# Performance work log

Hardware: AMD Instinct MI355X
Metric: run time of the kernel (lower is better)

Reference implementation:

```python
import jax, jax.numpy as jnp
import numpy as np

NUM_HEADS = 16
CLAMP = 1e4


def setup_inputs() -> dict:
    key = jax.random.key(0)
    ks = jax.random.split(key, 8)
    B, Nq, Nkv, Cq, Ckv = 4, 2048, 2048, 1024, 768
    s_q = 1.0 / np.sqrt(Cq)
    s_kv = 1.0 / np.sqrt(Ckv)
    return {
        "query": jax.random.normal(ks[0], (B, Nq, Cq), jnp.float32),
        "key_value": jax.random.normal(ks[1], (B, Nkv, Ckv), jnp.float32),
        "Wq": jax.random.normal(ks[2], (Cq, Cq), jnp.float32) * s_q,
        "bq": jnp.zeros((Cq,), jnp.float32),
        "Wk": jax.random.normal(ks[3], (Ckv, Cq), jnp.float32) * s_kv,
        "bk": jnp.zeros((Cq,), jnp.float32),
        "Wv": jax.random.normal(ks[4], (Ckv, Cq), jnp.float32) * s_kv,
        "bv": jnp.zeros((Cq,), jnp.float32),
        "Wo": jax.random.normal(ks[5], (Cq, Cq), jnp.float32) * s_q,
        "bo": jnp.zeros((Cq,), jnp.float32),
    }


def reference(query, key_value, Wq, bq, Wk, bk, Wv, bv, Wo, bo):
    B, Nq, Cq = query.shape
    Nkv = key_value.shape[1]
    H = NUM_HEADS
    D = Cq // H
    scale = D ** (-0.5)

    # projections -> [B, H, N, D]
    q = (query @ Wq + bq).reshape(B, Nq, H, D).transpose(0, 2, 1, 3)
    k = (key_value @ Wk + bk).reshape(B, Nkv, H, D).transpose(0, 2, 1, 3)
    v = (key_value @ Wv + bv).reshape(B, Nkv, H, D).transpose(0, 2, 1, 3)

    # scores [B, H, Nq, Nkv] with clamp (mask=None path)
    attn = jnp.einsum("bhqd,bhkd->bhqk", q, k) * scale
    attn = jnp.clip(attn, -CLAMP, CLAMP)
    attn = jax.nn.softmax(attn, axis=-1)
    # NaN fallback: replace with uniform attention if any NaN present
    attn = jnp.where(jnp.any(jnp.isnan(attn)),
                     jnp.asarray(1.0 / Nkv, attn.dtype), attn)

    # weighted sum -> [B, Nq, Cq]
    x = jnp.einsum("bhqk,bhkd->bqhd", attn, v).reshape(B, Nq, Cq)
    return x @ Wo + bo
```

## Files before the change

### kernel.cpp

```cpp
#include <hip/hip_runtime.h>
#include <hip/hip_bf16.h>
#include <stdint.h>


typedef unsigned short u16;
typedef __attribute__((ext_vector_type(2))) float f32x2;
typedef __attribute__((ext_vector_type(4))) short bf16x4;
typedef __attribute__((ext_vector_type(8))) short bf16x8;
typedef __attribute__((ext_vector_type(4))) float f32x4;
typedef __attribute__((ext_vector_type(16))) float f32x16;

__device__ __forceinline__ u16 f2bf(float x) {
  union { float f; uint32_t u; } c; c.f = x;
  uint32_t r = c.u + 0x7fffu + ((c.u >> 16) & 1u);
  return (u16)(r >> 16);
}

__device__ __forceinline__ uint32_t pkbf(float a, float b) {
#if __has_builtin(__builtin_amdgcn_cvt_pk_bf16_f32)
  typedef __attribute__((ext_vector_type(2))) __bf16 bf2;
  bf2 r = __builtin_amdgcn_cvt_pk_bf16_f32(a, b);
  return __builtin_bit_cast(uint32_t, r);
#else
  return (uint32_t)f2bf(a) | ((uint32_t)f2bf(b) << 16);
#endif
}

__device__ __forceinline__ void gld16(const void* g, void* l) {
  __builtin_amdgcn_global_load_lds(
      (const __attribute__((address_space(1))) void*)g,
      (__attribute__((address_space(3))) void*)l, 16, 0, 0);
}

__device__ __forceinline__ void cvt_body(const float* __restrict__ in,
                                         u16* __restrict__ out, int blk) {
  int i = (blk * 256 + threadIdx.x) * 8;
  float4 a = *(const float4*)(in + i);
  float4 b = *(const float4*)(in + i + 4);
  union { u16 u[8]; uint4 v; } o;
  o.u[0] = f2bf(a.x); o.u[1] = f2bf(a.y); o.u[2] = f2bf(a.z); o.u[3] = f2bf(a.w);
  o.u[4] = f2bf(b.x); o.u[5] = f2bf(b.y); o.u[6] = f2bf(b.z); o.u[7] = f2bf(b.w);
  *(uint4*)(out + i) = o.v;
}

__device__ __forceinline__ void transpose_body(const float* __restrict__ in,
                                               u16* __restrict__ out,
                                               int R, int C, int bx, int by) {
  __shared__ float tile[64][65];
  int c0 = bx * 64, r0 = by * 64;
  #pragma unroll
  for (int it = 0; it < 16; it++) {
    int idx = threadIdx.x + it * 256;
    int lr = idx >> 6, lc = idx & 63;
    tile[lr][lc] = in[(size_t)(r0 + lr) * C + c0 + lc];
  }
  __syncthreads();
  #pragma unroll
  for (int it = 0; it < 16; it++) {
    int idx = threadIdx.x + it * 256;
    int lc = idx >> 6, lr = idx & 63;
    out[(size_t)(c0 + lc) * R + r0 + lr] = f2bf(tile[lr][lc]);
  }
}

__global__ void prep_kernel(const float* __restrict__ query,
                            const float* __restrict__ key_value,
                            const float* __restrict__ Wq, const float* __restrict__ Wk,
                            const float* __restrict__ Wv, const float* __restrict__ Wo,
                            u16* qb, u16* kvb, u16* WqT, u16* WkT, u16* WvT, u16* WoT) {
  int blk = blockIdx.x;
  if (blk < 4096) { cvt_body(query, qb, blk); return; }
  if (blk < 7168) { cvt_body(key_value, kvb, blk - 4096); return; }
  if (blk < 7424) { int lo = blk - 7168; transpose_body(Wq, WqT, 1024, 1024, lo & 15, lo >> 4); return; }
  if (blk < 7616) { int lo = blk - 7424; transpose_body(Wk, WkT, 768, 1024, lo & 15, lo >> 4); return; }
  if (blk < 7808) { int lo = blk - 7616; transpose_body(Wv, WvT, 768, 1024, lo & 15, lo >> 4); return; }
  { int lo = blk - 7808; transpose_body(Wo, WoT, 1024, 1024, lo & 15, lo >> 4); return; }
}

template<bool SWAP>
__device__ __forceinline__ void gemm_kloop(const u16* __restrict__ A,
                                           const u16* __restrict__ BT,
                                           int K, char* smem, f32x4 (&acc)[4][4],
                                           int m0, int n0, int tid) {
  const u16* ap[4]; const u16* bp[4]; int ldA[4], ldB[4];
  #pragma unroll
  for (int it2 = 0; it2 < 4; it2++) {
    int s = it2 * 256 + tid;
    int row = s >> 3, cl = (s & 7) ^ (row & 7);
    ap[it2] = A + (size_t)(m0 + row) * K + cl * 8;
    bp[it2] = BT + (size_t)(n0 + row) * K + cl * 8;
    ldA[it2] = s * 16;
    ldB[it2] = 16384 + s * 16;
  }
  const int w = tid >> 6, l = tid & 63;
  const int lm = l & 15, lq = l >> 4;
  const int wr = w >> 1, wc = w & 1;
  int abase[4], bbase[4];
  #pragma unroll
  for (int i = 0; i < 4; i++) {
    int m = wr * 64 + i * 16 + lm;
    abase[i] = m * 128 + ((lq ^ (m & 7)) << 4);
    int n = wc * 64 + i * 16 + lm;
    bbase[i] = 16384 + n * 128 + ((lq ^ (n & 7)) << 4);
  }
  for (int k0 = 0; k0 < K; k0 += 64) {
    #pragma unroll
    for (int it2 = 0; it2 < 4; it2++) {
      gld16(ap[it2], smem + ldA[it2]);
      gld16(bp[it2], smem + ldB[it2]);
      ap[it2] += 64; bp[it2] += 64;
    }
    __syncthreads();
    #pragma unroll
    for (int kk = 0; kk < 2; kk++) {
      bf16x8 af[4], bf[4];
      #pragma unroll
      for (int i = 0; i < 4; i++)
        af[i] = *(const bf16x8*)(smem + (abase[i] ^ (kk << 6)));
      #pragma unroll
      for (int j = 0; j < 4; j++)
        bf[j] = *(const bf16x8*)(smem + (bbase[j] ^ (kk << 6)));
      #pragma unroll
      for (int i = 0; i < 4; i++)
        #pragma unroll
        for (int j = 0; j < 4; j++) {
          if (SWAP)
            acc[i][j] = __builtin_amdgcn_mfma_f32_16x16x32_bf16(bf[j], af[i], acc[i][j], 0, 0, 0);
          else
            acc[i][j] = __builtin_amdgcn_mfma_f32_16x16x32_bf16(af[i], bf[j], acc[i][j], 0, 0, 0);
        }
    }
    __syncthreads();
  }
}

__global__ __launch_bounds__(256, 3)
void gemm_qkv(const u16* __restrict__ qb, const u16* __restrict__ kvb,
              const u16* __restrict__ WqT, const u16* __restrict__ WkT,
              const u16* __restrict__ WvT,
              const float* __restrict__ bq, const float* __restrict__ bk,
              const float* __restrict__ bv,
              u16* __restrict__ Qb, u16* __restrict__ Kbf, u16* __restrict__ Vt,
              float qscale) {
  extern __shared__ __align__(16) char smem[];
  const int tid = threadIdx.x;
  const int w = tid >> 6, l = tid & 63;
  const int lm = l & 15, lq = l >> 4;
  const int m0 = blockIdx.y * 128, n0 = blockIdx.x * 128;
  const int wr = w >> 1, wc = w & 1;
  const int z = blockIdx.z;
  f32x4 acc[4][4] = {};

  u16* etile = (u16*)(smem + w * 9216);
  const int xr = l >> 3, cc = (l & 7) ^ xr;

  if (z < 2) {
    const u16* A = (z == 0) ? qb : kvb;
    const u16* BT = (z == 0) ? WqT : WkT;
    const float* bias = (z == 0) ? bq : bk;
    u16* out = (z == 0) ? Qb : Kbf;
    const float scale = (z == 0) ? qscale : 1.0f;
    const int K = (z == 0) ? 1024 : 768;
    gemm_kloop<true>(A, BT, K, smem, acc, m0, n0, tid);
    #pragma unroll
    for (int j = 0; j < 4; j++) {
      float4 b4 = *(const float4*)&bias[n0 + wc * 64 + j * 16 + lq * 4];
      #pragma unroll
      for (int i = 0; i < 4; i++) {
        uint2 pkd;
        pkd.x = pkbf((acc[i][j][0] + b4.x) * scale, (acc[i][j][1] + b4.y) * scale);
        pkd.y = pkbf((acc[i][j][2] + b4.z) * scale, (acc[i][j][3] + b4.w) * scale);
        *(uint2*)&etile[(i * 16 + lm) * 72 + j * 16 + lq * 4] = pkd;
      }
    }
    u16* gbase = out + (size_t)(m0 + wr * 64) * 1024 + n0 + wc * 64;
    #pragma unroll
    for (int co = 0; co < 8; co++) {
      int ml = co * 8 + xr;
      uint4 d = *(const uint4*)&etile[ml * 72 + cc * 8];
      *(uint4*)&gbase[(size_t)ml * 1024 + cc * 8] = d;
    }
  } else {
    gemm_kloop<false>(kvb, WvT, 768, smem, acc, m0, n0, tid);
    #pragma unroll
    for (int j = 0; j < 4; j++) {
      float bi = bv[n0 + wc * 64 + j * 16 + lm];
      #pragma unroll
      for (int i = 0; i < 4; i++) {
        uint2 pkd;
        pkd.x = pkbf(acc[i][j][0] + bi, acc[i][j][1] + bi);
        pkd.y = pkbf(acc[i][j][2] + bi, acc[i][j][3] + bi);
        *(uint2*)&etile[(j * 16 + lm) * 72 + i * 16 + lq * 4] = pkd;
      }
    }
    const int bb = m0 >> 11, mloc = (m0 & 2047) + wr * 64;
    u16* gbase = Vt + ((size_t)bb * 1024 + n0 + wc * 64) * 2048 + mloc;
    const int kvA = (cc >> 1) * 16 + (cc & 1) * 4;
    #pragma unroll
    for (int co = 0; co < 8; co++) {
      int dl = co * 8 + xr;
      uint2 dA = *(const uint2*)&etile[dl * 72 + kvA];
      uint2 dB = *(const uint2*)&etile[dl * 72 + kvA + 8];
      uint4 d = {dA.x, dA.y, dB.x, dB.y};
      *(uint4*)&gbase[(size_t)dl * 2048 + cc * 8] = d;
    }
  }
}

__global__ __launch_bounds__(256, 3)
void gemm_o(const u16* __restrict__ A, const u16* __restrict__ BT,
            const float* __restrict__ bias, float* __restrict__ Cout) {
  __shared__ __align__(16) char smem[32768];
  const int tid = threadIdx.x;
  const int w = tid >> 6, l = tid & 63;
  const int lm = l & 15, lq = l >> 4;
  const int m0 = blockIdx.y * 128, n0 = blockIdx.x * 128;
  const int wr = w >> 1, wc = w & 1;
  f32x4 acc[4][4] = {};
  gemm_kloop<false>(A, BT, 1024, smem, acc, m0, n0, tid);
  #pragma unroll
  for (int j = 0; j < 4; j++) {
    int gn = n0 + wc * 64 + j * 16 + lm;
    float bi = bias[gn];
    #pragma unroll
    for (int i = 0; i < 4; i++) {
      int gm = m0 + wr * 64 + i * 16 + lq * 4;
      #pragma unroll
      for (int r = 0; r < 4; r++)
        Cout[(size_t)(gm + r) * 1024 + gn] = acc[i][j][r] + bi;
    }
  }
}

__global__ __launch_bounds__(256, 2)
void attn_kernel(const u16* __restrict__ Q, const u16* __restrict__ Kb,
                 const u16* __restrict__ Vt, u16* __restrict__ X) {
  __shared__ __align__(16) char smem[32768];
  const int tid = threadIdx.x, w = tid >> 6, l = tid & 63;
  const int l31 = l & 31, h5 = l >> 5;
  const int bh = blockIdx.x, b = bh >> 4, h = bh & 15;
  const int q0 = blockIdx.y * 256 + w * 64;
  const int rx = l31 & 7;

  const u16* Kg = Kb + (size_t)b * 2048 * 1024 + h * 64;
  const u16* Vg = Vt + (size_t)bh * 64 * 2048;

  const u16 *kp0, *kp1, *vp0, *vp1;
  {
    int s = tid, r = s >> 3, c = (s & 7) ^ (r & 7);
    kp0 = Kg + (size_t)r * 1024 + c * 8;
    vp0 = Vg + (size_t)r * 2048 + c * 8;
    s = 256 + tid; r = s >> 3; c = (s & 7) ^ (r & 7);
    kp1 = Kg + (size_t)r * 1024 + c * 8;
    vp1 = Vg + (size_t)r * 2048 + c * 8;
  }
  const int kd0 = tid * 16, kd1 = (256 + tid) * 16;

  bf16x8 qfA[4], qfB[4];
  {
    const u16* qp = Q + ((size_t)(b * 2048 + q0 + l31)) * 1024 + h * 64 + h5 * 8;
    #pragma unroll
    for (int t = 0; t < 4; t++) qfA[t] = *(const bf16x8*)(qp + t * 16);
    qp += (size_t)32 * 1024;
    #pragma unroll
    for (int t = 0; t < 4; t++) qfB[t] = *(const bf16x8*)(qp + t * 16);
  }

  const int kvb2 = (l31 << 7) | ((rx ^ h5) << 4);
  const int vb2 = 16384 | (l31 << 7) | ((rx ^ h5) << 4);

  f32x16 xaccA[2] = {}, xaccB[2] = {};
  f32x2 lsA = {0.f, 0.f}, lsB = {0.f, 0.f};
  const f32x16 KZ = {};

  gld16(kp0, smem + kd0); gld16(kp1, smem + kd1);
  gld16(vp0, smem + 16384 + kd0); gld16(vp1, smem + 16384 + kd1);
  kp0 += 65536; kp1 += 65536; vp0 += 64; vp1 += 64;
  __syncthreads();

#define ATTN_STEP(CUR, DOPREF)                                                  \
  {                                                                             \
    if (DOPREF) {                                                               \
      const int nb = ((CUR) ^ 1) << 13;                                         \
      gld16(kp0, smem + nb + kd0); gld16(kp1, smem + nb + kd1);                 \
      gld16(vp0, smem + 16384 + nb + kd0); gld16(vp1, smem + 16384 + nb + kd1); \
      kp0 += 65536; kp1 += 65536; vp0 += 64; vp1 += 64;                         \
    }                                                                           \
    _Pragma("unroll")                                                           \
    for (int sub = 0; sub < 2; sub++) {                                         \
      const int km = ((CUR) << 13) | (sub << 12);                               \
      bf16x8 kf[4];                                                             \
      _Pragma("unroll")                                                         \
      for (int t = 0; t < 4; t++)                                               \
        kf[t] = *(const bf16x8*)(smem + (kvb2 ^ (km | (t << 5))));              \
      f32x16 st = __builtin_amdgcn_mfma_f32_32x32x16_bf16(kf[0], qfA[0], KZ, 0, 0, 0); \
      _Pragma("unroll")                                                         \
      for (int t = 1; t < 4; t++)                                               \
        st = __builtin_amdgcn_mfma_f32_32x32x16_bf16(kf[t], qfA[t], st, 0, 0, 0); \
      uint32_t pkA[8], pkB[8];                                                  \
      _Pragma("unroll")                                                         \
      for (int u = 0; u < 4; u++) {                                             \
        float p0 = __builtin_amdgcn_exp2f(st[4 * u + 0]);                       \
        float p1 = __builtin_amdgcn_exp2f(st[4 * u + 1]);                       \
        float p2 = __builtin_amdgcn_exp2f(st[4 * u + 2]);                       \
        float p3 = __builtin_amdgcn_exp2f(st[4 * u + 3]);                       \
        lsA += (f32x2){p0 + p2, p1 + p3};                                       \
        pkA[2 * u] = pkbf(p0, p1); pkA[2 * u + 1] = pkbf(p2, p3);               \
      }                                                                         \
      st = __builtin_amdgcn_mfma_f32_32x32x16_bf16(kf[0], qfB[0], KZ, 0, 0, 0); \
      _Pragma("unroll")                                                         \
      for (int t = 1; t < 4; t++)                                               \
        st = __builtin_amdgcn_mfma_f32_32x32x16_bf16(kf[t], qfB[t], st, 0, 0, 0); \
      _Pragma("unroll")                                                         \
      for (int u = 0; u < 4; u++) {                                             \
        float p0 = __builtin_amdgcn_exp2f(st[4 * u + 0]);                       \
        float p1 = __builtin_amdgcn_exp2f(st[4 * u + 1]);                       \
        float p2 = __builtin_amdgcn_exp2f(st[4 * u + 2]);                       \
        float p3 = __builtin_amdgcn_exp2f(st[4 * u + 3]);                       \
        lsB += (f32x2){p0 + p2, p1 + p3};                                       \
        pkB[2 * u] = pkbf(p0, p1); pkB[2 * u + 1] = pkbf(p2, p3);               \
      }                                                                         \
      _Pragma("unroll")                                                         \
      for (int c2 = 0; c2 < 2; c2++) {                                          \
        union { uint32_t d[4]; bf16x8 v; } pfA, pfB;                            \
        _Pragma("unroll")                                                       \
        for (int dd = 0; dd < 4; dd++) {                                        \
          pfA.d[dd] = pkA[4 * c2 + dd]; pfB.d[dd] = pkB[4 * c2 + dd];           \
        }                                                                       \
        const int vx = ((sub << 2) | (c2 << 1)) << 4;                           \
        _Pragma("unroll")                                                       \
        for (int dt = 0; dt < 2; dt++) {                                        \
          bf16x8 vf = *(const bf16x8*)(smem +                                   \
              (vb2 ^ (((CUR) << 13) | (dt << 12) | vx)));                       \
          xaccA[dt] = __builtin_amdgcn_mfma_f32_32x32x16_bf16(vf, pfA.v, xaccA[dt], 0, 0, 0); \
          xaccB[dt] = __builtin_amdgcn_mfma_f32_32x32x16_bf16(vf, pfB.v, xaccB[dt], 0, 0, 0); \
        }                                                                       \
      }                                                                         \
    }                                                                           \
    __syncthreads();                                                            \
  }

  for (int itp = 0; itp < 15; itp++) {
    ATTN_STEP(0, true)
    ATTN_STEP(1, true)
  }
  ATTN_STEP(0, true)
  ATTN_STEP(1, false)
#undef ATTN_STEP

  {
    float lsum = lsA[0] + lsA[1];
    const float inv = 1.0f / (lsum + __shfl_xor(lsum, 32));
    u16* xp = X + ((size_t)(b * 2048 + q0 + l31)) * 1024 + h * 64;
    #pragma unroll
    for (int dt = 0; dt < 2; dt++)
      #pragma unroll
      for (int g = 0; g < 4; g++) {
        const int d0 = dt * 32 + g * 8 + h5 * 4;
        uint2 o;
        o.x = pkbf(xaccA[dt][4 * g + 0] * inv, xaccA[dt][4 * g + 1] * inv);
        o.y = pkbf(xaccA[dt][4 * g + 2] * inv, xaccA[dt][4 * g + 3] * inv);
        *(uint2*)(xp + d0) = o;
      }
  }
  {
    float lsum = lsB[0] + lsB[1];
    const float inv = 1.0f / (lsum + __shfl_xor(lsum, 32));
    u16* xp = X + ((size_t)(b * 2048 + q0 + 32 + l31)) * 1024 + h * 64;
    #pragma unroll
    for (int dt = 0; dt < 2; dt++)
      #pragma unroll
      for (int g = 0; g < 4; g++) {
        const int d0 = dt * 32 + g * 8 + h5 * 4;
        uint2 o;
        o.x = pkbf(xaccB[dt][4 * g + 0] * inv, xaccB[dt][4 * g + 1] * inv);
        o.y = pkbf(xaccB[dt][4 * g + 2] * inv, xaccB[dt][4 * g + 3] * inv);
        *(uint2*)(xp + d0) = o;
      }
  }
}

extern "C" void kernel_launch(void* const* d_in, const int* in_sizes, int n_in,
                              void* d_out, int out_size, void* d_ws, size_t ws_size,
                              hipStream_t stream) {
  const float* query     = (const float*)d_in[0];
  const float* key_value = (const float*)d_in[1];
  const float* Wq = (const float*)d_in[2];
  const float* bq = (const float*)d_in[3];
  const float* Wk = (const float*)d_in[4];
  const float* bk = (const float*)d_in[5];
  const float* Wv = (const float*)d_in[6];
  const float* bv = (const float*)d_in[7];
  const float* Wo = (const float*)d_in[8];
  const float* bo = (const float*)d_in[9];
  float* out = (float*)d_out;

  char* ws = (char*)d_ws;
  size_t off = 0;
  auto alloc = [&](size_t bytes) -> void* {
    void* p = ws + off; off += (bytes + 255) & ~(size_t)255; return p;
  };
  u16* qb  = (u16*)alloc((size_t)8192 * 1024 * 2);
  u16* kvb = (u16*)alloc((size_t)8192 * 768 * 2);
  u16* WqT = (u16*)alloc((size_t)1024 * 1024 * 2);
  u16* WkT = (u16*)alloc((size_t)1024 * 768 * 2);
  u16* WvT = (u16*)alloc((size_t)1024 * 768 * 2);
  u16* WoT = (u16*)alloc((size_t)1024 * 1024 * 2);
  u16* Qb  = (u16*)alloc((size_t)8192 * 1024 * 2);
  u16* Kbf = (u16*)alloc((size_t)8192 * 1024 * 2);
  u16* Vt  = (u16*)alloc((size_t)8192 * 1024 * 2);
  u16* Xb  = (u16*)alloc((size_t)8192 * 1024 * 2);

  prep_kernel<<<8064, 256, 0, stream>>>(query, key_value, Wq, Wk, Wv, Wo,
                                        qb, kvb, WqT, WkT, WvT, WoT);

  const float qscale = 0.125f * 1.4426950408889634f;
  gemm_qkv<<<dim3(8, 64, 3), 256, 36864, stream>>>(qb, kvb, WqT, WkT, WvT,
                                                   bq, bk, bv, Qb, Kbf, Vt, qscale);

  attn_kernel<<<dim3(64, 8), 256, 0, stream>>>(Qb, Kbf, Vt, Xb);

  gemm_o<<<dim3(8, 64), 256, 0, stream>>>(Xb, WoT, bo, out);
}
```

Before: 291.0 us.

## Store K/V in MFMA fragment layout and load attention operands directly to registers

The QKV GEMM epilogue now writes K and V in a per-head, fragment-ordered layout so each lane can read its MFMA operand with contiguous 16-byte global loads. The attention kernel drops its shared-memory staging, LDS swizzle and per-step barriers, and instead double-buffers K/V fragments in registers with a software-prefetched global load of the next tile. Each wave now fetches K/V independently from global or L2, where before they were shared through LDS. Register pressure also rises.

```diff
diff --git a/kernel.cpp b/kernel.cpp
--- a/kernel.cpp
+++ b/kernel.cpp
@@ -140,7 +140,7 @@
               const u16* __restrict__ WvT,
               const float* __restrict__ bq, const float* __restrict__ bk,
               const float* __restrict__ bv,
-              u16* __restrict__ Qb, u16* __restrict__ Kbf, u16* __restrict__ Vt,
+              u16* __restrict__ Qb, u16* __restrict__ Kf, u16* __restrict__ Vf,
               float qscale) {
   extern __shared__ __align__(16) char smem[];
   const int tid = threadIdx.x;
@@ -158,7 +158,6 @@
     const u16* A = (z == 0) ? qb : kvb;
     const u16* BT = (z == 0) ? WqT : WkT;
     const float* bias = (z == 0) ? bq : bk;
-    u16* out = (z == 0) ? Qb : Kbf;
     const float scale = (z == 0) ? qscale : 1.0f;
     const int K = (z == 0) ? 1024 : 768;
     gemm_kloop<true>(A, BT, K, smem, acc, m0, n0, tid);
@@ -173,12 +172,24 @@
         *(uint2*)&etile[(i * 16 + lm) * 72 + j * 16 + lq * 4] = pkd;
       }
     }
-    u16* gbase = out + (size_t)(m0 + wr * 64) * 1024 + n0 + wc * 64;
-    #pragma unroll
-    for (int co = 0; co < 8; co++) {
-      int ml = co * 8 + xr;
-      uint4 d = *(const uint4*)&etile[ml * 72 + cc * 8];
-      *(uint4*)&gbase[(size_t)ml * 1024 + cc * 8] = d;
+    if (z == 0) {
+      u16* gbase = Qb + (size_t)(m0 + wr * 64) * 1024 + n0 + wc * 64;
+      #pragma unroll
+      for (int co = 0; co < 8; co++) {
+        int ml = co * 8 + xr;
+        uint4 d = *(const uint4*)&etile[ml * 72 + cc * 8];
+        *(uint4*)&gbase[(size_t)ml * 1024 + cc * 8] = d;
+      }
+    } else {
+      const int kvg = m0 + wr * 64;
+      const int bh_ = ((kvg >> 11) << 4) + ((n0 + wc * 64) >> 6);
+      u16* gK = Kf + (size_t)bh_ * 131072 + (size_t)((kvg & 2047) >> 5) * 2048;
+      #pragma unroll
+      for (int co = 0; co < 8; co++) {
+        int ml = co * 8 + xr;
+        uint4 d = *(const uint4*)&etile[ml * 72 + cc * 8];
+        *(uint4*)&gK[(ml >> 5) * 2048 + cc * 256 + (ml & 31) * 8] = d;
+      }
     }
   } else {
     gemm_kloop<false>(kvb, WvT, 768, smem, acc, m0, n0, tid);
@@ -193,8 +204,9 @@
         *(uint2*)&etile[(j * 16 + lm) * 72 + i * 16 + lq * 4] = pkd;
       }
     }
-    const int bb = m0 >> 11, mloc = (m0 & 2047) + wr * 64;
-    u16* gbase = Vt + ((size_t)bb * 1024 + n0 + wc * 64) * 2048 + mloc;
+    const int bh_ = ((m0 >> 11) << 4) + ((n0 + wc * 64) >> 6);
+    const int wt = ((m0 & 2047) + wr * 64) >> 6;
+    u16* gV = Vf + (size_t)bh_ * 131072 + (size_t)wt * 4096;
     const int kvA = (cc >> 1) * 16 + (cc & 1) * 4;
     #pragma unroll
     for (int co = 0; co < 8; co++) {
@@ -202,7 +214,7 @@
       uint2 dA = *(const uint2*)&etile[dl * 72 + kvA];
       uint2 dB = *(const uint2*)&etile[dl * 72 + kvA + 8];
       uint4 d = {dA.x, dA.y, dB.x, dB.y};
-      *(uint4*)&gbase[(size_t)dl * 2048 + cc * 8] = d;
+      *(uint4*)&gV[cc * 512 + dl * 8] = d;
     }
   }
 }
@@ -232,29 +244,67 @@
   }
 }
 
+template<bool PREF>
+__device__ __forceinline__ void attn_step(
+    const u16*& kp, const u16*& vp,
+    const bf16x8 (&kc)[4], const bf16x8 (&vc)[4],
+    bf16x8 (&kn)[4], bf16x8 (&vn)[4],
+    const bf16x8 (&qfA)[4], const bf16x8 (&qfB)[4],
+    f32x16 (&xA)[2], f32x16 (&xB)[2], f32x2& lsA, f32x2& lsB) {
+  if (PREF) {
+    #pragma unroll
+    for (int t = 0; t < 4; t++) kn[t] = *(const bf16x8*)(kp + t * 512);
+    #pragma unroll
+    for (int c2 = 0; c2 < 2; c2++)
+      #pragma unroll
+      for (int dt = 0; dt < 2; dt++)
+        vn[c2 * 2 + dt] = *(const bf16x8*)(vp + c2 * 1024 + dt * 256);
+    kp += 2048; vp += 2048;
+  }
+  const f32x16 KZ = {};
+  f32x16 stA = __builtin_amdgcn_mfma_f32_32x32x16_bf16(kc[0], qfA[0], KZ, 0, 0, 0);
+  f32x16 stB = __builtin_amdgcn_mfma_f32_32x32x16_bf16(kc[0], qfB[0], KZ, 0, 0, 0);
+  #pragma unroll
+  for (int t = 1; t < 4; t++) {
+    stA = __builtin_amdgcn_mfma_f32_32x32x16_bf16(kc[t], qfA[t], stA, 0, 0, 0);
+    stB = __builtin_amdgcn_mfma_f32_32x32x16_bf16(kc[t], qfB[t], stB, 0, 0, 0);
+  }
+  uint32_t pkA[8], pkB[8];
+  #pragma unroll
+  for (int u = 0; u < 4; u++) {
+    float a0 = __builtin_amdgcn_exp2f(stA[4 * u + 0]);
+    float a1 = __builtin_amdgcn_exp2f(stA[4 * u + 1]);
+    float a2 = __builtin_amdgcn_exp2f(stA[4 * u + 2]);
+    float a3 = __builtin_amdgcn_exp2f(stA[4 * u + 3]);
+    lsA += (f32x2){a0 + a2, a1 + a3};
+    pkA[2 * u] = pkbf(a0, a1); pkA[2 * u + 1] = pkbf(a2, a3);
+    float b0 = __builtin_amdgcn_exp2f(stB[4 * u + 0]);
+    float b1 = __builtin_amdgcn_exp2f(stB[4 * u + 1]);
+    float b2 = __builtin_amdgcn_exp2f(stB[4 * u + 2]);
+    float b3 = __builtin_amdgcn_exp2f(stB[4 * u + 3]);
+    lsB += (f32x2){b0 + b2, b1 + b3};
+    pkB[2 * u] = pkbf(b0, b1); pkB[2 * u + 1] = pkbf(b2, b3);
+  }
+  #pragma unroll
+  for (int c2 = 0; c2 < 2; c2++) {
+    union { uint32_t d[4]; bf16x8 v; } pfA, pfB;
+    #pragma unroll
+    for (int dd = 0; dd < 4; dd++) { pfA.d[dd] = pkA[4 * c2 + dd]; pfB.d[dd] = pkB[4 * c2 + dd]; }
+    #pragma unroll
+    for (int dt = 0; dt < 2; dt++) {
+      xA[dt] = __builtin_amdgcn_mfma_f32_32x32x16_bf16(vc[c2 * 2 + dt], pfA.v, xA[dt], 0, 0, 0);
+      xB[dt] = __builtin_amdgcn_mfma_f32_32x32x16_bf16(vc[c2 * 2 + dt], pfB.v, xB[dt], 0, 0, 0);
+    }
+  }
+}
+
 __global__ __launch_bounds__(256, 2)
-void attn_kernel(const u16* __restrict__ Q, const u16* __restrict__ Kb,
-                 const u16* __restrict__ Vt, u16* __restrict__ X) {
-  __shared__ __align__(16) char smem[32768];
+void attn_kernel(const u16* __restrict__ Q, const u16* __restrict__ Kf,
+                 const u16* __restrict__ Vf, u16* __restrict__ X) {
   const int tid = threadIdx.x, w = tid >> 6, l = tid & 63;
   const int l31 = l & 31, h5 = l >> 5;
   const int bh = blockIdx.x, b = bh >> 4, h = bh & 15;
   const int q0 = blockIdx.y * 256 + w * 64;
-  const int rx = l31 & 7;
-
-  const u16* Kg = Kb + (size_t)b * 2048 * 1024 + h * 64;
-  const u16* Vg = Vt + (size_t)bh * 64 * 2048;
-
-  const u16 *kp0, *kp1, *vp0, *vp1;
-  {
-    int s = tid, r = s >> 3, c = (s & 7) ^ (r & 7);
-    kp0 = Kg + (size_t)r * 1024 + c * 8;
-    vp0 = Vg + (size_t)r * 2048 + c * 8;
-    s = 256 + tid; r = s >> 3; c = (s & 7) ^ (r & 7);
-    kp1 = Kg + (size_t)r * 1024 + c * 8;
-    vp1 = Vg + (size_t)r * 2048 + c * 8;
-  }
-  const int kd0 = tid * 16, kd1 = (256 + tid) * 16;
 
   bf16x8 qfA[4], qfB[4];
   {
@@ -266,87 +316,28 @@
     for (int t = 0; t < 4; t++) qfB[t] = *(const bf16x8*)(qp + t * 16);
   }
 
-  const int kvb2 = (l31 << 7) | ((rx ^ h5) << 4);
-  const int vb2 = 16384 | (l31 << 7) | ((rx ^ h5) << 4);
-
-  f32x16 xaccA[2] = {}, xaccB[2] = {};
+  const u16* kp = Kf + (size_t)bh * 131072 + h5 * 256 + l31 * 8;
+  const u16* vp = Vf + (size_t)bh * 131072 + h5 * 512 + l31 * 8;
+
+  f32x16 xA[2] = {}, xB[2] = {};
   f32x2 lsA = {0.f, 0.f}, lsB = {0.f, 0.f};
-  const f32x16 KZ = {};
-
-  gld16(kp0, smem + kd0); gld16(kp1, smem + kd1);
-  gld16(vp0, smem + 16384 + kd0); gld16(vp1, smem + 16384 + kd1);
-  kp0 += 65536; kp1 += 65536; vp0 += 64; vp1 += 64;
-  __syncthreads();
-
-#define ATTN_STEP(CUR, DOPREF)                                                  \
-  {                                                                             \
-    if (DOPREF) {                                                               \
-      const int nb = ((CUR) ^ 1) << 13;                                         \
-      gld16(kp0, smem + nb + kd0); gld16(kp1, smem + nb + kd1);                 \
-      gld16(vp0, smem + 16384 + nb + kd0); gld16(vp1, smem + 16384 + nb + kd1); \
-      kp0 += 65536; kp1 += 65536; vp0 += 64; vp1 += 64;                         \
-    }                                                                           \
-    _Pragma("unroll")                                                           \
-    for (int sub = 0; sub < 2; sub++) {                                         \
-      const int km = ((CUR) << 13) | (sub << 12);                               \
-      bf16x8 kf[4];                                                             \
-      _Pragma("unroll")                                                         \
-      for (int t = 0; t < 4; t++)                                               \
-        kf[t] = *(const bf16x8*)(smem + (kvb2 ^ (km | (t << 5))));              \
-      f32x16 st = __builtin_amdgcn_mfma_f32_32x32x16_bf16(kf[0], qfA[0], KZ, 0, 0, 0); \
-      _Pragma("unroll")                                                         \
-      for (int t = 1; t < 4; t++)                                               \
-        st = __builtin_amdgcn_mfma_f32_32x32x16_bf16(kf[t], qfA[t], st, 0, 0, 0); \
-      uint32_t pkA[8], pkB[8];                                                  \
-      _Pragma("unroll")                                                         \
-      for (int u = 0; u < 4; u++) {                                             \
-        float p0 = __builtin_amdgcn_exp2f(st[4 * u + 0]);                       \
-        float p1 = __builtin_amdgcn_exp2f(st[4 * u + 1]);                       \
-        float p2 = __builtin_amdgcn_exp2f(st[4 * u + 2]);                       \
-        float p3 = __builtin_amdgcn_exp2f(st[4 * u + 3]);                       \
-        lsA += (f32x2){p0 + p2, p1 + p3};                                       \
-        pkA[2 * u] = pkbf(p0, p1); pkA[2 * u + 1] = pkbf(p2, p3);               \
-      }                                                                         \
-      st = __builtin_amdgcn_mfma_f32_32x32x16_bf16(kf[0], qfB[0], KZ, 0, 0, 0); \
-      _Pragma("unroll")                                                         \
-      for (int t = 1; t < 4; t++)                                               \
-        st = __builtin_amdgcn_mfma_f32_32x32x16_bf16(kf[t], qfB[t], st, 0, 0, 0); \
-      _Pragma("unroll")                                                         \
-      for (int u = 0; u < 4; u++) {                                             \
-        float p0 = __builtin_amdgcn_exp2f(st[4 * u + 0]);                       \
-        float p1 = __builtin_amdgcn_exp2f(st[4 * u + 1]);                       \
-        float p2 = __builtin_amdgcn_exp2f(st[4 * u + 2]);                       \
-        float p3 = __builtin_amdgcn_exp2f(st[4 * u + 3]);                       \
-        lsB += (f32x2){p0 + p2, p1 + p3};                                       \
-        pkB[2 * u] = pkbf(p0, p1); pkB[2 * u + 1] = pkbf(p2, p3);               \
-      }                                                                         \
-      _Pragma("unroll")                                                         \
-      for (int c2 = 0; c2 < 2; c2++) {                                          \
-        union { uint32_t d[4]; bf16x8 v; } pfA, pfB;                            \
-        _Pragma("unroll")                                                       \
-        for (int dd = 0; dd < 4; dd++) {                                        \
-          pfA.d[dd] = pkA[4 * c2 + dd]; pfB.d[dd] = pkB[4 * c2 + dd];           \
-        }                                                                       \
-        const int vx = ((sub << 2) | (c2 << 1)) << 4;                           \
-        _Pragma("unroll")                                                       \
-        for (int dt = 0; dt < 2; dt++) {                                        \
-          bf16x8 vf = *(const bf16x8*)(smem +                                   \
-              (vb2 ^ (((CUR) << 13) | (dt << 12) | vx)));                       \
-          xaccA[dt] = __builtin_amdgcn_mfma_f32_32x32x16_bf16(vf, pfA.v, xaccA[dt], 0, 0, 0); \
-          xaccB[dt] = __builtin_amdgcn_mfma_f32_32x32x16_bf16(vf, pfB.v, xaccB[dt], 0, 0, 0); \
-        }                                                                       \
-      }                                                                         \
-    }                                                                           \
-    __syncthreads();                                                            \
-  }
-
-  for (int itp = 0; itp < 15; itp++) {
-    ATTN_STEP(0, true)
-    ATTN_STEP(1, true)
-  }
-  ATTN_STEP(0, true)
-  ATTN_STEP(1, false)
-#undef ATTN_STEP
+
+  bf16x8 KA[4], VA[4], KB[4], VB[4];
+  #pragma unroll
+  for (int t = 0; t < 4; t++) KA[t] = *(const bf16x8*)(kp + t * 512);
+  #pragma unroll
+  for (int c2 = 0; c2 < 2; c2++)
+    #pragma unroll
+    for (int dt = 0; dt < 2; dt++)
+      VA[c2 * 2 + dt] = *(const bf16x8*)(vp + c2 * 1024 + dt * 256);
+  kp += 2048; vp += 2048;
+
+  for (int s2 = 0; s2 < 31; s2++) {
+    attn_step<true>(kp, vp, KA, VA, KB, VB, qfA, qfB, xA, xB, lsA, lsB);
+    attn_step<true>(kp, vp, KB, VB, KA, VA, qfA, qfB, xA, xB, lsA, lsB);
+  }
+  attn_step<true>(kp, vp, KA, VA, KB, VB, qfA, qfB, xA, xB, lsA, lsB);
+  attn_step<false>(kp, vp, KB, VB, KA, VA, qfA, qfB, xA, xB, lsA, lsB);
 
   {
     float lsum = lsA[0] + lsA[1];
@@ -358,8 +349,8 @@
       for (int g = 0; g < 4; g++) {
         const int d0 = dt * 32 + g * 8 + h5 * 4;
         uint2 o;
-        o.x = pkbf(xaccA[dt][4 * g + 0] * inv, xaccA[dt][4 * g + 1] * inv);
-        o.y = pkbf(xaccA[dt][4 * g + 2] * inv, xaccA[dt][4 * g + 3] * inv);
+        o.x = pkbf(xA[dt][4 * g + 0] * inv, xA[dt][4 * g + 1] * inv);
+        o.y = pkbf(xA[dt][4 * g + 2] * inv, xA[dt][4 * g + 3] * inv);
         *(uint2*)(xp + d0) = o;
       }
   }
@@ -373,8 +364,8 @@
       for (int g = 0; g < 4; g++) {
         const int d0 = dt * 32 + g * 8 + h5 * 4;
         uint2 o;
-        o.x = pkbf(xaccB[dt][4 * g + 0] * inv, xaccB[dt][4 * g + 1] * inv);
-        o.y = pkbf(xaccB[dt][4 * g + 2] * inv, xaccB[dt][4 * g + 3] * inv);
+        o.x = pkbf(xB[dt][4 * g + 0] * inv, xB[dt][4 * g + 1] * inv);
+        o.y = pkbf(xB[dt][4 * g + 2] * inv, xB[dt][4 * g + 3] * inv);
         *(uint2*)(xp + d0) = o;
       }
   }
@@ -407,8 +398,8 @@
   u16* WvT = (u16*)alloc((size_t)1024 * 768 * 2);
   u16* WoT = (u16*)alloc((size_t)1024 * 1024 * 2);
   u16* Qb  = (u16*)alloc((size_t)8192 * 1024 * 2);
-  u16* Kbf = (u16*)alloc((size_t)8192 * 1024 * 2);
-  u16* Vt  = (u16*)alloc((size_t)8192 * 1024 * 2);
+  u16* Kf  = (u16*)alloc((size_t)8192 * 1024 * 2);
+  u16* Vf  = (u16*)alloc((size_t)8192 * 1024 * 2);
   u16* Xb  = (u16*)alloc((size_t)8192 * 1024 * 2);
 
   prep_kernel<<<8064, 256, 0, stream>>>(query, key_value, Wq, Wk, Wv, Wo,
@@ -416,9 +407,9 @@
 
   const float qscale = 0.125f * 1.4426950408889634f;
   gemm_qkv<<<dim3(8, 64, 3), 256, 36864, stream>>>(qb, kvb, WqT, WkT, WvT,
-                                                   bq, bk, bv, Qb, Kbf, Vt, qscale);
-
-  attn_kernel<<<dim3(64, 8), 256, 0, stream>>>(Qb, Kbf, Vt, Xb);
+                                                   bq, bk, bv, Qb, Kf, Vf, qscale);
+
+  attn_kernel<<<dim3(64, 8), 256, 0, stream>>>(Qb, Kf, Vf, Xb);
 
   gemm_o<<<dim3(8, 64), 256, 0, stream>>>(Xb, WoT, bo, out);
 }
```

Result: no change. 291.0 us (+0.0%).
